# Kernel optimization log

Measured on AMD Instinct MI355X. Metric: run time of the kernel, lower is better.

The kernel has to match this reference:

```python
import jax, jax.numpy as jnp
import numpy as np

B, S, D, H = 2, 2048, 1024, 16
HD = D // H  # head dim = 64

def setup_inputs() -> dict:
    key = jax.random.key(0)
    ks = jax.random.split(key, 3)
    scale = 1.0 / np.sqrt(D)
    return {
        "x": jax.random.normal(ks[0], (B, S, D), jnp.float32),
        "W_attn": jax.random.normal(ks[1], (D, 3 * D), jnp.float32) * scale,
        "b_attn": jnp.zeros((3 * D,), jnp.float32),
        "W_proj": jax.random.normal(ks[2], (D, D), jnp.float32) * scale,
        "b_proj": jnp.zeros((D,), jnp.float32),
    }

def reference(x, W_attn, b_attn, W_proj, b_proj):
    b, s, d = x.shape
    qkv = x @ W_attn + b_attn                      # [B,S,3D]
    q, k, v = jnp.split(qkv, 3, axis=-1)
    # [B,S,D] -> [B,H,S,HD]
    def heads(t):
        return t.reshape(b, s, H, HD).transpose(0, 2, 1, 3)
    q, k, v = heads(q), heads(k), heads(v)
    scores = jnp.einsum('bhqd,bhkd->bhqk', q, k) * (1.0 / np.sqrt(HD))
    causal = jnp.tril(jnp.ones((s, s), dtype=bool))
    scores = jnp.where(causal[None, None], scores, -jnp.inf)
    probs = jax.nn.softmax(scores, axis=-1)
    y = jnp.einsum('bhqk,bhkd->bhqd', probs, v)    # [B,H,S,HD]
    y = y.transpose(0, 2, 1, 3).reshape(b, s, d)
    return y @ W_proj + b_proj
```

## Files before the change

### kernel.cpp

```cpp
#include <hip/hip_runtime.h>

typedef __bf16 bf16;
typedef __bf16 bf16x4 __attribute__((ext_vector_type(4)));
typedef __bf16 bf16x8 __attribute__((ext_vector_type(8)));
typedef float f32x4 __attribute__((ext_vector_type(4)));

#define S_LEN 2048
#define D_DIM 1024
#define N_HEAD 16
#define HEAD_DIM 64
#define M_TOK 4096
#define BH 32

#define EXP2F(x) __builtin_amdgcn_exp2f(x)
#define Q_SCALE 0.18033688f

#define SW(r, c) ((c) ^ (((r) & 3) << 4))
#define SIG(r) (((r) & 0x23) | (((r) & 0x04) << 2) | (((r) & 0x18) >> 1))

typedef __attribute__((address_space(3))) void lds_void;
typedef const __attribute__((address_space(1))) void gbl_void;

__device__ __forceinline__ void gl_lds16(const bf16* g, bf16* l) {
  __builtin_amdgcn_global_load_lds((gbl_void*)g, (lds_void*)l, 16, 0, 0);
}

__global__ __launch_bounds__(256) void k_cast(const float* __restrict__ x,
                                              bf16* __restrict__ o, int n) {
  int i = (blockIdx.x * 256 + threadIdx.x) * 4;
  if (i >= n) return;
  float4 v = *(const float4*)(x + i);
  bf16x4 w;
  w[0] = (bf16)v.x; w[1] = (bf16)v.y; w[2] = (bf16)v.z; w[3] = (bf16)v.w;
  *(bf16x4*)(o + i) = w;
}

__global__ __launch_bounds__(256) void k_transpose(const float* __restrict__ W,
                                                   bf16* __restrict__ Wt,
                                                   int K, int N) {
  __shared__ float tile[32][33];
  int nb = blockIdx.x, kb = blockIdx.y;
  int t = threadIdx.x;
  int r = t >> 3, c4 = (t & 7) * 4;
  float4 v = *(const float4*)&W[(kb * 32 + r) * N + nb * 32 + c4];
  tile[r][c4 + 0] = v.x; tile[r][c4 + 1] = v.y;
  tile[r][c4 + 2] = v.z; tile[r][c4 + 3] = v.w;
  __syncthreads();
  bf16x4 o;
  #pragma unroll
  for (int i = 0; i < 4; i++) o[i] = (bf16)tile[c4 + i][r];
  *(bf16x4*)&Wt[(nb * 32 + r) * K + kb * 32 + c4] = o;
}

__global__ __launch_bounds__(256, 2)
void k_gemm_qkv(const bf16* __restrict__ A, const bf16* __restrict__ Bt,
                const float* __restrict__ bias,
                bf16* __restrict__ qk, bf16* __restrict__ vT) {
  __shared__ bf16 As[128 * 32];
  __shared__ bf16 Bs[128 * 32];
  const int K = 1024;
  int bn = blockIdx.x, bm = blockIdx.y;
  int t = threadIdx.x;
  int wave = t >> 6, lane = t & 63, c = lane & 15, quad = lane >> 4;
  int wm = wave & 1, wn = wave >> 1;
  int ldrow = lane >> 2, ldcol = (lane & 3) * 8;

  const bf16* Ag = A + (size_t)(bm * 128) * K;
  const bf16* Bg = Bt + (size_t)(bn * 128) * K;

  f32x4 acc[4][4] = {};

  for (int k0 = 0; k0 < K; k0 += 32) {
    __syncthreads();
    #pragma unroll
    for (int q = 0; q < 2; q++) {
      int r0 = (wave * 2 + q) * 16;
      gl_lds16(&Ag[(size_t)(r0 + ldrow) * K + k0 + ldcol], &As[r0 * 32]);
      gl_lds16(&Bg[(size_t)(r0 + ldrow) * K + k0 + ldcol], &Bs[r0 * 32]);
    }
    __syncthreads();
    bf16x8 af[4];
    #pragma unroll
    for (int mt = 0; mt < 4; mt++)
      af[mt] = *(const bf16x8*)&As[(wm * 64 + mt * 16 + c) * 32 + quad * 8];
    #pragma unroll
    for (int nt = 0; nt < 4; nt++) {
      bf16x8 bfr = *(const bf16x8*)&Bs[(wn * 64 + nt * 16 + c) * 32 + quad * 8];
      #pragma unroll
      for (int mt = 0; mt < 4; mt++)
        acc[mt][nt] = __builtin_amdgcn_mfma_f32_16x16x32_bf16(af[mt], bfr, acc[mt][nt], 0, 0, 0);
    }
  }

  #pragma unroll
  for (int nt = 0; nt < 4; nt++) {
    int n = bn * 128 + wn * 64 + nt * 16 + c;
    int which = n >> 10, nl = n & 1023;
    int h = nl >> 6, hd = nl & 63;
    float bv = bias[n];
    #pragma unroll
    for (int mt = 0; mt < 4; mt++) {
      int m0 = bm * 128 + wm * 64 + mt * 16 + quad * 4;
      int b = m0 >> 11, s0 = m0 & 2047;
      int bh = b * N_HEAD + h;
      if (which == 2) {
        bf16x4 o;
        #pragma unroll
        for (int r = 0; r < 4; r++) o[r] = (bf16)(acc[mt][nt][r] + bv);
        *(bf16x4*)&vT[((size_t)bh * HEAD_DIM + hd) * S_LEN + s0] = o;
      } else if (which == 0) {
        #pragma unroll
        for (int r = 0; r < 4; r++)
          qk[(bh * S_LEN + s0 + r) * HEAD_DIM + hd] = (bf16)((acc[mt][nt][r] + bv) * Q_SCALE);
      } else {
        #pragma unroll
        for (int r = 0; r < 4; r++)
          qk[BH * S_LEN * HEAD_DIM + (bh * S_LEN + s0 + r) * HEAD_DIM + hd] = (bf16)(acc[mt][nt][r] + bv);
      }
    }
  }
}

__global__ __launch_bounds__(512, 4)
void k_attn(const bf16* __restrict__ qk, const bf16* __restrict__ vT,
            bf16* __restrict__ y) {
  __shared__ bf16 Ks[2][64][64];
  __shared__ bf16 Vs[2][64][64];
  int bx = blockIdx.x;
  int bh = bx & 31;
  int p = bx >> 5;
  int t = threadIdx.x, w = t >> 6, lane = t & 63, c = lane & 15, quad = lane >> 4;
  int strip = w >> 2, wr = w & 3;
  int myTile = strip ? (31 - p) : p;
  const bf16* Qg = qk + (size_t)bh * (S_LEN * HEAD_DIM);
  const bf16* Kg = qk + (size_t)(BH + bh) * (S_LEN * HEAD_DIM);
  const bf16* Vg = vT + (size_t)bh * (HEAD_DIM * S_LEN);
  int b = bh >> 4, h = bh & 15;
  int srow = t >> 3, scol = (t & 7) * 8;
  int swcol = SW(srow, scol);
  int sigr = SIG(srow);

  const int nkb = 32 - p;
  const int myLast = strip ? (31 - p) : p;
  const int dthr = wr * 16 + c;

  bf16x8 qf[2];
  f32x4 acc[4] = {};
  float mM = -1e30f, lL = 0.f;
  {
    int qr = myTile * 64 + wr * 16 + c;
    qf[0] = *(const bf16x8*)&Qg[qr * HEAD_DIM + quad * 8];
    qf[1] = *(const bf16x8*)&Qg[qr * HEAD_DIM + 32 + quad * 8];
  }

  bf16x8 kr = *(const bf16x8*)&Kg[srow * HEAD_DIM + scol];
  bf16x8 vr = *(const bf16x8*)&Vg[(size_t)srow * S_LEN + scol];
  *(bf16x8*)&Ks[0][sigr][swcol] = kr;
  *(bf16x8*)&Vs[0][srow][swcol] = vr;

  for (int kb = 0; kb < nkb; kb++) {
    __syncthreads();
    int cur = kb & 1;
    bool haveNext = (kb + 1 < nkb);
    if (haveNext) {
      kr = *(const bf16x8*)&Kg[((kb + 1) * 64 + srow) * HEAD_DIM + scol];
      vr = *(const bf16x8*)&Vg[(size_t)srow * S_LEN + (kb + 1) * 64 + scol];
    }

    bool act = (kb <= myLast);
    if (act) {
      bool dia = (kb == myLast);

      f32x4 sc[4];
      __builtin_amdgcn_s_setprio(1);
      #pragma unroll
      for (int kt = 0; kt < 4; kt++) {
        int krr = kt * 16 + c;
        bf16x8 kf0 = *(const bf16x8*)&Ks[cur][krr][SW(krr, quad * 8)];
        bf16x8 kf1 = *(const bf16x8*)&Ks[cur][krr][SW(krr, 32 + quad * 8)];
        f32x4 z = {};
        z = __builtin_amdgcn_mfma_f32_16x16x32_bf16(kf0, qf[0], z, 0, 0, 0);
        z = __builtin_amdgcn_mfma_f32_16x16x32_bf16(kf1, qf[1], z, 0, 0, 0);
        sc[kt] = z;
      }
      __builtin_amdgcn_s_setprio(0);

      if (dia) {
        #pragma unroll
        for (int kt = 0; kt < 4; kt++) {
          int kbase = (kt >> 1) * 32 + quad * 8 + (kt & 1) * 4;
          #pragma unroll
          for (int r = 0; r < 4; r++)
            if (kbase + r > dthr) sc[kt][r] = -1e30f;
        }
      }

      bf16x8 pf[2];
      {
        float mx = sc[0][0];
        #pragma unroll
        for (int kt = 0; kt < 4; kt++)
          #pragma unroll
          for (int r = 0; r < 4; r++) mx = fmaxf(mx, sc[kt][r]);
        mx = fmaxf(mx, __shfl_xor(mx, 16));
        mx = fmaxf(mx, __shfl_xor(mx, 32));
        float mnew = fmaxf(mM, mx);
        float alpha = EXP2F(mM - mnew);
        float sum = 0.f;
        #pragma unroll
        for (int kt = 0; kt < 4; kt++) {
          #pragma unroll
          for (int r = 0; r < 4; r++) {
            float pv = EXP2F(sc[kt][r] - mnew);
            sum += pv;
            pf[kt >> 1][(kt & 1) * 4 + r] = (bf16)pv;
          }
        }
        sum += __shfl_xor(sum, 16);
        sum += __shfl_xor(sum, 32);
        lL = lL * alpha + sum;
        mM = mnew;
        #pragma unroll
        for (int dt = 0; dt < 4; dt++)
          #pragma unroll
          for (int r = 0; r < 4; r++) acc[dt][r] *= alpha;
      }

      __builtin_amdgcn_s_setprio(1);
      #pragma unroll
      for (int ks = 0; ks < 2; ks++) {
        #pragma unroll
        for (int dt = 0; dt < 4; dt++) {
          int vrow = dt * 16 + c;
          bf16x8 vf = *(const bf16x8*)&Vs[cur][vrow][SW(vrow, ks * 32 + quad * 8)];
          acc[dt] = __builtin_amdgcn_mfma_f32_16x16x32_bf16(vf, pf[ks], acc[dt], 0, 0, 0);
        }
      }
      __builtin_amdgcn_s_setprio(0);
    }

    if (haveNext) {
      int nxt = cur ^ 1;
      *(bf16x8*)&Ks[nxt][sigr][swcol] = kr;
      *(bf16x8*)&Vs[nxt][srow][swcol] = vr;
    }
  }

  {
    int q = myTile * 64 + wr * 16 + c;
    float linv = 1.0f / lL;
    #pragma unroll
    for (int dt = 0; dt < 4; dt++) {
      bf16x4 o;
      #pragma unroll
      for (int r = 0; r < 4; r++) o[r] = (bf16)(acc[dt][r] * linv);
      *(bf16x4*)&y[((size_t)(b * S_LEN + q) * N_HEAD + h) * HEAD_DIM + dt * 16 + quad * 4] = o;
    }
  }
}

__global__ __launch_bounds__(256, 2)
void k_gemm_proj(const bf16* __restrict__ A, const bf16* __restrict__ Bt,
                 const float* __restrict__ bias, float* __restrict__ out) {
  __shared__ bf16 As[128 * 32];
  __shared__ bf16 Bs[64 * 32];
  const int K = 1024;
  int bn = blockIdx.x, bm = blockIdx.y;
  int t = threadIdx.x;
  int wave = t >> 6, lane = t & 63, c = lane & 15, quad = lane >> 4;
  int wm = wave & 1, wn = wave >> 1;
  int ldrow = lane >> 2, ldcol = (lane & 3) * 8;

  const bf16* Ag = A + (size_t)(bm * 128) * K;
  const bf16* Bg = Bt + (size_t)(bn * 64) * K;

  f32x4 acc[4][2] = {};

  for (int k0 = 0; k0 < K; k0 += 32) {
    __syncthreads();
    #pragma unroll
    for (int q = 0; q < 2; q++) {
      int r0 = (wave * 2 + q) * 16;
      gl_lds16(&Ag[(size_t)(r0 + ldrow) * K + k0 + ldcol], &As[r0 * 32]);
    }
    gl_lds16(&Bg[(size_t)(wave * 16 + ldrow) * K + k0 + ldcol], &Bs[wave * 16 * 32]);
    __syncthreads();
    bf16x8 af[4];
    #pragma unroll
    for (int mt = 0; mt < 4; mt++)
      af[mt] = *(const bf16x8*)&As[(wm * 64 + mt * 16 + c) * 32 + quad * 8];
    #pragma unroll
    for (int nt = 0; nt < 2; nt++) {
      bf16x8 bfr = *(const bf16x8*)&Bs[(wn * 32 + nt * 16 + c) * 32 + quad * 8];
      #pragma unroll
      for (int mt = 0; mt < 4; mt++)
        acc[mt][nt] = __builtin_amdgcn_mfma_f32_16x16x32_bf16(af[mt], bfr, acc[mt][nt], 0, 0, 0);
    }
  }

  #pragma unroll
  for (int nt = 0; nt < 2; nt++) {
    int n = bn * 64 + wn * 32 + nt * 16 + c;
    float bv = bias[n];
    #pragma unroll
    for (int mt = 0; mt < 4; mt++) {
      #pragma unroll
      for (int r = 0; r < 4; r++) {
        int m = bm * 128 + wm * 64 + mt * 16 + quad * 4 + r;
        out[(size_t)m * D_DIM + n] = acc[mt][nt][r] + bv;
      }
    }
  }
}

extern "C" void kernel_launch(void* const* d_in, const int* in_sizes, int n_in,
                              void* d_out, int out_size, void* d_ws, size_t ws_size,
                              hipStream_t stream) {
  const float* x      = (const float*)d_in[0];
  const float* W_attn = (const float*)d_in[1];
  const float* b_attn = (const float*)d_in[2];
  const float* W_proj = (const float*)d_in[3];
  const float* b_proj = (const float*)d_in[4];
  float* out = (float*)d_out;

  bf16* x_bf = (bf16*)d_ws;
  bf16* wat  = x_bf + 4096 * 1024;
  bf16* wpt  = wat + 3072 * 1024;
  bf16* qk   = wpt + 1024 * 1024;
  bf16* vT   = qk + 8 * 1024 * 1024;
  bf16* y_bf = vT + 4 * 1024 * 1024;

  k_cast<<<4096, 256, 0, stream>>>(x, x_bf, 4096 * 1024);
  k_transpose<<<dim3(3072 / 32, 1024 / 32), 256, 0, stream>>>(W_attn, wat, 1024, 3072);
  k_transpose<<<dim3(1024 / 32, 1024 / 32), 256, 0, stream>>>(W_proj, wpt, 1024, 1024);
  k_gemm_qkv<<<dim3(24, 32), 256, 0, stream>>>(x_bf, wat, b_attn, qk, vT);
  k_attn<<<512, 512, 0, stream>>>(qk, vT, y_bf);
  k_gemm_proj<<<dim3(16, 32), 256, 0, stream>>>(y_bf, wpt, b_proj, out);
}
```

Baseline: 181.7 us.

## Software-pipeline QK^T one tile ahead, lazy softmax rescale, reorder attention blocks

The attention loop now computes the next K tile's scores (S=QK^T) while running softmax and PV on the current tile. K is prefetched two tiles ahead and V one tile ahead, with K and V on separate buffer phases. The online softmax skips rescaling the accumulator unless the row max grows by more than a threshold, and the row max and sum reductions use tree order. The second half of the grid is assigned tiles in reverse order to balance the causal workload. This costs extra score registers and a slightly more complex buffer schedule.

Result: no change. 184.1 us (+1.3%).

```diff
diff --git a/kernel.cpp b/kernel.cpp
--- a/kernel.cpp
+++ b/kernel.cpp
@@ -14,6 +14,7 @@
 
 #define EXP2F(x) __builtin_amdgcn_exp2f(x)
 #define Q_SCALE 0.18033688f
+#define RESCALE_THR 8.0f
 
 #define SW(r, c) ((c) ^ (((r) & 3) << 4))
 #define SIG(r) (((r) & 0x23) | (((r) & 0x04) << 2) | (((r) & 0x18) >> 1))
@@ -127,8 +128,9 @@
   __shared__ bf16 Ks[2][64][64];
   __shared__ bf16 Vs[2][64][64];
   int bx = blockIdx.x;
-  int bh = bx & 31;
-  int p = bx >> 5;
+  int bh, p;
+  if (bx < 256) { bh = bx & 31; p = bx >> 5; }
+  else          { int j = bx - 256; bh = j & 31; p = 15 - (j >> 5); }
   int t = threadIdx.x, w = t >> 6, lane = t & 63, c = lane & 15, quad = lane >> 4;
   int strip = w >> 2, wr = w & 3;
   int myTile = strip ? (31 - p) : p;
@@ -153,77 +155,101 @@
     qf[1] = *(const bf16x8*)&Qg[qr * HEAD_DIM + 32 + quad * 8];
   }
 
-  bf16x8 kr = *(const bf16x8*)&Kg[srow * HEAD_DIM + scol];
-  bf16x8 vr = *(const bf16x8*)&Vg[(size_t)srow * S_LEN + scol];
-  *(bf16x8*)&Ks[0][sigr][swcol] = kr;
-  *(bf16x8*)&Vs[0][srow][swcol] = vr;
+  {
+    bf16x8 k0 = *(const bf16x8*)&Kg[srow * HEAD_DIM + scol];
+    bf16x8 v0 = *(const bf16x8*)&Vg[(size_t)srow * S_LEN + scol];
+    *(bf16x8*)&Ks[0][sigr][swcol] = k0;
+    *(bf16x8*)&Vs[0][srow][swcol] = v0;
+  }
+  bf16x8 kr = *(const bf16x8*)&Kg[(64 + srow) * HEAD_DIM + scol];
+  bf16x8 vr;
+  __syncthreads();
+
+  f32x4 scC[4], scN[4];
+  __builtin_amdgcn_s_setprio(1);
+  #pragma unroll
+  for (int kt = 0; kt < 4; kt++) {
+    int krr = kt * 16 + c;
+    bf16x8 kf0 = *(const bf16x8*)&Ks[0][krr][SW(krr, quad * 8)];
+    bf16x8 kf1 = *(const bf16x8*)&Ks[0][krr][SW(krr, 32 + quad * 8)];
+    f32x4 z = {};
+    z = __builtin_amdgcn_mfma_f32_16x16x32_bf16(kf0, qf[0], z, 0, 0, 0);
+    z = __builtin_amdgcn_mfma_f32_16x16x32_bf16(kf1, qf[1], z, 0, 0, 0);
+    scC[kt] = z;
+  }
+  __builtin_amdgcn_s_setprio(0);
+  *(bf16x8*)&Ks[1][sigr][swcol] = kr;
 
   for (int kb = 0; kb < nkb; kb++) {
     __syncthreads();
     int cur = kb & 1;
-    bool haveNext = (kb + 1 < nkb);
-    if (haveNext) {
-      kr = *(const bf16x8*)&Kg[((kb + 1) * 64 + srow) * HEAD_DIM + scol];
-      vr = *(const bf16x8*)&Vg[(size_t)srow * S_LEN + (kb + 1) * 64 + scol];
-    }
-
-    bool act = (kb <= myLast);
-    if (act) {
-      bool dia = (kb == myLast);
-
-      f32x4 sc[4];
+    bool haveK2 = (kb + 2 < nkb);
+    bool haveV1 = (kb + 1 < nkb);
+    if (haveK2) kr = *(const bf16x8*)&Kg[((kb + 2) * 64 + srow) * HEAD_DIM + scol];
+    if (haveV1) vr = *(const bf16x8*)&Vg[(size_t)srow * S_LEN + (kb + 1) * 64 + scol];
+
+    if (kb + 1 <= myLast) {
       __builtin_amdgcn_s_setprio(1);
       #pragma unroll
       for (int kt = 0; kt < 4; kt++) {
         int krr = kt * 16 + c;
-        bf16x8 kf0 = *(const bf16x8*)&Ks[cur][krr][SW(krr, quad * 8)];
-        bf16x8 kf1 = *(const bf16x8*)&Ks[cur][krr][SW(krr, 32 + quad * 8)];
+        bf16x8 kf0 = *(const bf16x8*)&Ks[cur ^ 1][krr][SW(krr, quad * 8)];
+        bf16x8 kf1 = *(const bf16x8*)&Ks[cur ^ 1][krr][SW(krr, 32 + quad * 8)];
         f32x4 z = {};
         z = __builtin_amdgcn_mfma_f32_16x16x32_bf16(kf0, qf[0], z, 0, 0, 0);
         z = __builtin_amdgcn_mfma_f32_16x16x32_bf16(kf1, qf[1], z, 0, 0, 0);
-        sc[kt] = z;
+        scN[kt] = z;
       }
       __builtin_amdgcn_s_setprio(0);
-
-      if (dia) {
+    }
+
+    if (kb <= myLast) {
+      if (kb == myLast) {
         #pragma unroll
         for (int kt = 0; kt < 4; kt++) {
           int kbase = (kt >> 1) * 32 + quad * 8 + (kt & 1) * 4;
           #pragma unroll
           for (int r = 0; r < 4; r++)
-            if (kbase + r > dthr) sc[kt][r] = -1e30f;
+            if (kbase + r > dthr) scC[kt][r] = -1e30f;
         }
       }
 
       bf16x8 pf[2];
       {
-        float mx = sc[0][0];
+        float tm[4];
+        #pragma unroll
+        for (int kt = 0; kt < 4; kt++)
+          tm[kt] = fmaxf(fmaxf(scC[kt][0], scC[kt][1]), fmaxf(scC[kt][2], scC[kt][3]));
+        float mx = fmaxf(fmaxf(tm[0], tm[1]), fmaxf(tm[2], tm[3]));
+        mx = fmaxf(mx, __shfl_xor(mx, 16));
+        mx = fmaxf(mx, __shfl_xor(mx, 32));
+        if (!__all(mx <= mM + RESCALE_THR)) {
+          float mnew = fmaxf(mM, mx);
+          float alpha = EXP2F(mM - mnew);
+          lL *= alpha;
+          #pragma unroll
+          for (int dt = 0; dt < 4; dt++)
+            #pragma unroll
+            for (int r = 0; r < 4; r++) acc[dt][r] *= alpha;
+          mM = mnew;
+        }
+        float pv[16];
         #pragma unroll
         for (int kt = 0; kt < 4; kt++)
           #pragma unroll
-          for (int r = 0; r < 4; r++) mx = fmaxf(mx, sc[kt][r]);
-        mx = fmaxf(mx, __shfl_xor(mx, 16));
-        mx = fmaxf(mx, __shfl_xor(mx, 32));
-        float mnew = fmaxf(mM, mx);
-        float alpha = EXP2F(mM - mnew);
-        float sum = 0.f;
-        #pragma unroll
-        for (int kt = 0; kt < 4; kt++) {
-          #pragma unroll
           for (int r = 0; r < 4; r++) {
-            float pv = EXP2F(sc[kt][r] - mnew);
-            sum += pv;
-            pf[kt >> 1][(kt & 1) * 4 + r] = (bf16)pv;
+            float e = EXP2F(scC[kt][r] - mM);
+            pv[kt * 4 + r] = e;
+            pf[kt >> 1][(kt & 1) * 4 + r] = (bf16)e;
           }
-        }
+        float s0 = (pv[0] + pv[1]) + (pv[2] + pv[3]);
+        float s1 = (pv[4] + pv[5]) + (pv[6] + pv[7]);
+        float s2 = (pv[8] + pv[9]) + (pv[10] + pv[11]);
+        float s3 = (pv[12] + pv[13]) + (pv[14] + pv[15]);
+        float sum = (s0 + s1) + (s2 + s3);
         sum += __shfl_xor(sum, 16);
         sum += __shfl_xor(sum, 32);
-        lL = lL * alpha + sum;
-        mM = mnew;
-        #pragma unroll
-        for (int dt = 0; dt < 4; dt++)
-          #pragma unroll
-          for (int r = 0; r < 4; r++) acc[dt][r] *= alpha;
+        lL += sum;
       }
 
       __builtin_amdgcn_s_setprio(1);
@@ -239,11 +265,11 @@
       __builtin_amdgcn_s_setprio(0);
     }
 
-    if (haveNext) {
-      int nxt = cur ^ 1;
-      *(bf16x8*)&Ks[nxt][sigr][swcol] = kr;
-      *(bf16x8*)&Vs[nxt][srow][swcol] = vr;
-    }
+    if (haveK2) *(bf16x8*)&Ks[cur][sigr][swcol] = kr;
+    if (haveV1) *(bf16x8*)&Vs[cur ^ 1][srow][swcol] = vr;
+
+    #pragma unroll
+    for (int kt = 0; kt < 4; kt++) scC[kt] = scN[kt];
   }
 
   {
```

## Use 128-key blocks with direct global-to-LDS loads in causal attention

Applied to the files above, without the earlier changes.

The attention kernel now processes keys in 128-wide blocks instead of 64, halving the number of loop iterations and block barriers. K/V tiles are loaded with global_load_lds directly into the swizzled LDS layout, using an inverse row permutation, so the register staging and LDS store are removed. Block-to-tile mapping is also remapped for blocks beyond 256 to balance causal work, and the softmax reductions are restructured into trees. LDS usage doubles and causal masking now wastes more work on the diagonal block, which may hurt occupancy at 4 blocks per CU.

Measured after the change: 175.5 us. 3.4% less time.

```diff
diff --git a/kernel.cpp b/kernel.cpp
--- a/kernel.cpp
+++ b/kernel.cpp
@@ -17,6 +17,7 @@
 
 #define SW(r, c) ((c) ^ (((r) & 3) << 4))
 #define SIG(r) (((r) & 0x23) | (((r) & 0x04) << 2) | (((r) & 0x18) >> 1))
+#define SIGINV(y) (((y) & 0x23) | (((y) >> 2) & 0x04) | (((y) & 0x0C) << 1))
 
 typedef __attribute__((address_space(3))) void lds_void;
 typedef const __attribute__((address_space(1))) void gbl_void;
@@ -124,11 +125,12 @@
 __global__ __launch_bounds__(512, 4)
 void k_attn(const bf16* __restrict__ qk, const bf16* __restrict__ vT,
             bf16* __restrict__ y) {
-  __shared__ bf16 Ks[2][64][64];
-  __shared__ bf16 Vs[2][64][64];
+  __shared__ bf16 Ks[2][128][64];
+  __shared__ bf16 Vs[2][64][128];
   int bx = blockIdx.x;
-  int bh = bx & 31;
-  int p = bx >> 5;
+  int bh, p;
+  if (bx < 256) { bh = bx & 31; p = bx >> 5; }
+  else          { int j = bx - 256; bh = j & 31; p = 15 - (j >> 5); }
   int t = threadIdx.x, w = t >> 6, lane = t & 63, c = lane & 15, quad = lane >> 4;
   int strip = w >> 2, wr = w & 3;
   int myTile = strip ? (31 - p) : p;
@@ -136,13 +138,27 @@
   const bf16* Kg = qk + (size_t)(BH + bh) * (S_LEN * HEAD_DIM);
   const bf16* Vg = vT + (size_t)bh * (HEAD_DIM * S_LEN);
   int b = bh >> 4, h = bh & 15;
-  int srow = t >> 3, scol = (t & 7) * 8;
-  int swcol = SW(srow, scol);
-  int sigr = SIG(srow);
-
-  const int nkb = 32 - p;
-  const int myLast = strip ? (31 - p) : p;
-  const int dthr = wr * 16 + c;
+
+  const int NKB2 = ((31 - p) >> 1) + 1;
+  const int myLast2 = myTile >> 1;
+  const int dmask = wr * 16 + c + ((myTile & 1) << 6);
+
+  int jK0 = w * 16 + (lane >> 3);
+  int jK1 = jK0 + 8;
+  int cK  = ((lane & 7) * 8) ^ ((jK0 & 3) << 4);
+  int kRow0 = ((jK0 >> 6) << 6) + SIGINV(jK0 & 63);
+  int kRow1 = ((jK1 >> 6) << 6) + SIGINV(jK1 & 63);
+  const bf16* kSrc0 = Kg + (size_t)kRow0 * HEAD_DIM + cK;
+  const bf16* kSrc1 = Kg + (size_t)kRow1 * HEAD_DIM + cK;
+  int jV0 = w * 8 + (lane >> 4);
+  int cV  = ((lane & 15) * 8) ^ ((jV0 & 3) << 4);
+  const bf16* vSrc0 = Vg + (size_t)jV0 * S_LEN + cV;
+  const bf16* vSrc1 = vSrc0 + (size_t)4 * S_LEN;
+
+  gl_lds16(kSrc0, &Ks[0][w * 16][0]);
+  gl_lds16(kSrc1, &Ks[0][w * 16 + 8][0]);
+  gl_lds16(vSrc0, &Vs[0][w * 8][0]);
+  gl_lds16(vSrc1, &Vs[0][w * 8 + 4][0]);
 
   bf16x8 qf[2];
   f32x4 acc[4] = {};
@@ -153,28 +169,23 @@
     qf[1] = *(const bf16x8*)&Qg[qr * HEAD_DIM + 32 + quad * 8];
   }
 
-  bf16x8 kr = *(const bf16x8*)&Kg[srow * HEAD_DIM + scol];
-  bf16x8 vr = *(const bf16x8*)&Vg[(size_t)srow * S_LEN + scol];
-  *(bf16x8*)&Ks[0][sigr][swcol] = kr;
-  *(bf16x8*)&Vs[0][srow][swcol] = vr;
-
-  for (int kb = 0; kb < nkb; kb++) {
-    __syncthreads();
-    int cur = kb & 1;
-    bool haveNext = (kb + 1 < nkb);
-    if (haveNext) {
-      kr = *(const bf16x8*)&Kg[((kb + 1) * 64 + srow) * HEAD_DIM + scol];
-      vr = *(const bf16x8*)&Vg[(size_t)srow * S_LEN + (kb + 1) * 64 + scol];
-    }
-
-    bool act = (kb <= myLast);
-    if (act) {
-      bool dia = (kb == myLast);
-
-      f32x4 sc[4];
+  for (int kb2 = 0; kb2 < NKB2; kb2++) {
+    __syncthreads();
+    int cur = kb2 & 1, nxt = cur ^ 1;
+    if (kb2 + 1 < NKB2) {
+      size_t ko = (size_t)(kb2 + 1) * (128 * HEAD_DIM);
+      int    vo = (kb2 + 1) * 128;
+      gl_lds16(kSrc0 + ko, &Ks[nxt][w * 16][0]);
+      gl_lds16(kSrc1 + ko, &Ks[nxt][w * 16 + 8][0]);
+      gl_lds16(vSrc0 + vo, &Vs[nxt][w * 8][0]);
+      gl_lds16(vSrc1 + vo, &Vs[nxt][w * 8 + 4][0]);
+    }
+
+    if (kb2 <= myLast2) {
+      f32x4 sc[8];
       __builtin_amdgcn_s_setprio(1);
       #pragma unroll
-      for (int kt = 0; kt < 4; kt++) {
+      for (int kt = 0; kt < 8; kt++) {
         int krr = kt * 16 + c;
         bf16x8 kf0 = *(const bf16x8*)&Ks[cur][krr][SW(krr, quad * 8)];
         bf16x8 kf1 = *(const bf16x8*)&Ks[cur][krr][SW(krr, 32 + quad * 8)];
@@ -185,50 +196,54 @@
       }
       __builtin_amdgcn_s_setprio(0);
 
-      if (dia) {
-        #pragma unroll
-        for (int kt = 0; kt < 4; kt++) {
-          int kbase = (kt >> 1) * 32 + quad * 8 + (kt & 1) * 4;
+      if (kb2 == myLast2) {
+        #pragma unroll
+        for (int kt = 0; kt < 8; kt++) {
+          int kbase = ((kt >> 2) << 6) + (((kt >> 1) & 1) << 5) + quad * 8 + ((kt & 1) << 2);
           #pragma unroll
           for (int r = 0; r < 4; r++)
-            if (kbase + r > dthr) sc[kt][r] = -1e30f;
+            if (kbase + r > dmask) sc[kt][r] = -1e30f;
         }
       }
 
-      bf16x8 pf[2];
+      bf16x8 pf[4];
       {
-        float mx = sc[0][0];
-        #pragma unroll
-        for (int kt = 0; kt < 4; kt++)
-          #pragma unroll
-          for (int r = 0; r < 4; r++) mx = fmaxf(mx, sc[kt][r]);
+        float tm[8];
+        #pragma unroll
+        for (int kt = 0; kt < 8; kt++)
+          tm[kt] = fmaxf(fmaxf(sc[kt][0], sc[kt][1]), fmaxf(sc[kt][2], sc[kt][3]));
+        float mx = fmaxf(fmaxf(fmaxf(tm[0], tm[1]), fmaxf(tm[2], tm[3])),
+                         fmaxf(fmaxf(tm[4], tm[5]), fmaxf(tm[6], tm[7])));
         mx = fmaxf(mx, __shfl_xor(mx, 16));
         mx = fmaxf(mx, __shfl_xor(mx, 32));
         float mnew = fmaxf(mM, mx);
         float alpha = EXP2F(mM - mnew);
-        float sum = 0.f;
-        #pragma unroll
-        for (int kt = 0; kt < 4; kt++) {
-          #pragma unroll
-          for (int r = 0; r < 4; r++) {
-            float pv = EXP2F(sc[kt][r] - mnew);
-            sum += pv;
-            pf[kt >> 1][(kt & 1) * 4 + r] = (bf16)pv;
-          }
-        }
-        sum += __shfl_xor(sum, 16);
-        sum += __shfl_xor(sum, 32);
-        lL = lL * alpha + sum;
         mM = mnew;
+        lL *= alpha;
         #pragma unroll
         for (int dt = 0; dt < 4; dt++)
           #pragma unroll
           for (int r = 0; r < 4; r++) acc[dt][r] *= alpha;
+        float ss[4] = {0.f, 0.f, 0.f, 0.f};
+        #pragma unroll
+        for (int kt = 0; kt < 8; kt++) {
+          float e0 = EXP2F(sc[kt][0] - mM), e1 = EXP2F(sc[kt][1] - mM);
+          float e2 = EXP2F(sc[kt][2] - mM), e3 = EXP2F(sc[kt][3] - mM);
+          pf[kt >> 1][(kt & 1) * 4 + 0] = (bf16)e0;
+          pf[kt >> 1][(kt & 1) * 4 + 1] = (bf16)e1;
+          pf[kt >> 1][(kt & 1) * 4 + 2] = (bf16)e2;
+          pf[kt >> 1][(kt & 1) * 4 + 3] = (bf16)e3;
+          ss[kt & 3] += (e0 + e1) + (e2 + e3);
+        }
+        float sum = (ss[0] + ss[1]) + (ss[2] + ss[3]);
+        sum += __shfl_xor(sum, 16);
+        sum += __shfl_xor(sum, 32);
+        lL += sum;
       }
 
       __builtin_amdgcn_s_setprio(1);
       #pragma unroll
-      for (int ks = 0; ks < 2; ks++) {
+      for (int ks = 0; ks < 4; ks++) {
         #pragma unroll
         for (int dt = 0; dt < 4; dt++) {
           int vrow = dt * 16 + c;
@@ -237,12 +252,6 @@
         }
       }
       __builtin_amdgcn_s_setprio(0);
-    }
-
-    if (haveNext) {
-      int nxt = cur ^ 1;
-      *(bf16x8*)&Ks[nxt][sigr][swcol] = kr;
-      *(bf16x8*)&Vs[nxt][srow][swcol] = vr;
     }
   }
 
```
